# Performance work log

Measured on AMD Instinct MI355X. Metric: run time of the kernel, lower is better.

Reference implementation:

```python
import jax, jax.numpy as jnp
import numpy as np

N_EMB = 512
DIM = 64
BETA = 0.25
EPS = 1e-10


def setup_inputs() -> dict:
    key = jax.random.key(0)
    k1, k2 = jax.random.split(key)
    z = jax.random.normal(k1, (32, 64, 64, 64), dtype=jnp.float32)  # (B, C=DIM, H, W)
    # embedding weight initialized uniform(-1/K, 1/K) as in the module
    weight = jax.random.uniform(k2, (N_EMB, DIM), dtype=jnp.float32,
                                minval=-1.0 / N_EMB, maxval=1.0 / N_EMB)
    return {"z": z, "weight": weight}


def reference(z, weight):
    # (B,C,H,W) -> (B,H,W,C)
    zp = jnp.transpose(z, (0, 2, 3, 1))
    zf = zp.reshape(-1, DIM)  # (N, D)
    # pairwise squared distances ||z||^2 + ||e||^2 - 2 z.e  -> (N, K)
    d = (jnp.sum(zf * zf, axis=1, keepdims=True)
         + jnp.sum(weight * weight, axis=1)
         - 2.0 * zf @ weight.T)
    codebook = jnp.argmin(d, axis=1)  # (N,)
    encodings = jax.nn.one_hot(codebook, N_EMB, dtype=zf.dtype)  # (N, K)
    # direct gather == one_hot @ weight (same math, efficient form)
    z_q = weight[codebook].reshape(zp.shape)
    sg = jax.lax.stop_gradient
    loss = jnp.mean((sg(z_q) - zp) ** 2) + BETA * jnp.mean((z_q - sg(zp)) ** 2)
    # straight-through estimator
    z_q = zp + sg(z_q - zp)
    e_mean = jnp.mean(encodings, axis=0)
    perplexity = jnp.exp(-jnp.sum(e_mean * jnp.log(e_mean + EPS)))
    z_q = jnp.transpose(z_q, (0, 3, 1, 2))  # back to (B,C,H,W)
    return (loss, z_q, perplexity, encodings, codebook)
```

## Files before the change

### kernel.cpp

```cpp
#include <hip/hip_runtime.h>
#include <math.h>

#define NK 512
#define NPTS (32*64*64)
#define NELEM (32*64*64*64)

#define OFF_LOSS 0
#define OFF_ZQ   1
#define OFF_PERP (1 + NELEM)
#define OFF_ENC  (2 + NELEM)
#define OFF_CB   (2 + NELEM + (size_t)NPTS * NK)


__global__ __launch_bounds__(256) void vq_prep(const float* __restrict__ wg,
                                               float* __restrict__ wTT,
                                               float* __restrict__ bnd) {
    __shared__ float tl[64 * 65];
    const int t = threadIdx.x;
    const int kbase = blockIdx.x * 64;
    #pragma unroll
    for (int it = 0; it < 16; ++it) {
        int i = it * 256 + t;
        int k = i >> 6, d = i & 63;
        tl[k * 65 + d] = wg[(size_t)(kbase + k) * 64 + d];
    }
    __syncthreads();
    #pragma unroll
    for (int it = 0; it < 16; ++it) {
        int i = it * 256 + t;
        int kk = i & 63, d = i >> 6;
        int k = kbase + kk;
        wTT[(size_t)((k >> 3) * 64 + d) * 8 + (k & 7)] = tl[kk * 65 + d];
    }
    if (t < 64) {
        float s = 0.f;
        #pragma unroll 4
        for (int d = 0; d < 64; ++d) {
            float v = tl[t * 65 + d];
            s = __fadd_rn(s, __fmul_rn(v, v));
        }
        bnd[kbase + t] = s;
    }
}

__global__ __launch_bounds__(256, 4) void vq_fused(const float* __restrict__ zg,
                                                   const float* __restrict__ wg,
                                                   const float* __restrict__ wTT,
                                                   const float* __restrict__ bndg,
                                                   float* __restrict__ out,
                                                   int* __restrict__ hist,
                                                   double* __restrict__ lossAcc) {
    const int t = threadIdx.x;
    const int wave = t >> 6;
    const int lane = t & 63;
    const int rowInBlk = wave >> 1;
    const int half = wave & 1;
    const int r = blockIdx.x * 2 + rowInBlk;
    const int b = r >> 6;
    const int h = r & 63;
    const size_t base = (size_t)b * 262144 + (size_t)h * 64;

    __shared__ float shv[4][64];
    __shared__ int   shi[4][64];
    __shared__ int   shm[2][64];

    float zreg[64];
    #pragma unroll
    for (int d = 0; d < 64; ++d)
        zreg[d] = zg[base + (size_t)d * 4096 + lane];

    float a = 0.f;
    #pragma unroll
    for (int d = 0; d < 64; ++d)
        a = __fadd_rn(a, __fmul_rn(zreg[d], zreg[d]));

    const int shalf = __builtin_amdgcn_readfirstlane(half);
    const float* wbase = wTT + (size_t)shalf * 32 * 512;
    const float* bnb = bndg + shalf * 256;

    float best = INFINITY;
    int bidx = 0;

    #pragma unroll 1
    for (int cc = 0; cc < 32; ++cc) {
        const float* wrow = wbase + cc * 512;
        float acc[8];
        #pragma unroll
        for (int j = 0; j < 8; ++j) acc[j] = 0.f;

        #pragma unroll
        for (int d = 0; d < 64; ++d) {
            const float zv = zreg[d];
            #pragma unroll
            for (int j = 0; j < 8; ++j)
                acc[j] = fmaf(zv, wrow[d * 8 + j], acc[j]);
        }

        #pragma unroll
        for (int j = 0; j < 8; ++j) {
            float dist = __fsub_rn(__fadd_rn(a, bnb[cc * 8 + j]), 2.0f * acc[j]);
            int k = shalf * 256 + cc * 8 + j;
            if (dist < best) { best = dist; bidx = k; }
        }
    }

    shv[wave][lane] = best;
    shi[wave][lane] = bidx;
    __syncthreads();
    const int w0 = rowInBlk * 2;
    float v0 = shv[w0][lane];     int i0 = shi[w0][lane];
    float v1 = shv[w0 + 1][lane]; int i1 = shi[w0 + 1][lane];
    const int mi = (v1 < v0) ? i1 : i0;

    if (half == 0) {
        shm[rowInBlk][lane] = mi;
        out[OFF_CB + (size_t)r * 64 + lane] = (float)mi;
        atomicAdd(&hist[mi], 1);
    }
    __syncthreads();

    {
        float* encb = out + OFF_ENC + ((size_t)r * 64) * 512;
        const int e0 = lane * 4;
        #pragma unroll 4
        for (int p = 0; p < 32; ++p) {
            int pt = shalf * 32 + p;
            int idx = shm[rowInBlk][pt];
            float* erow = encb + (size_t)pt * 512;
            float4 A, B;
            A.x = (e0 + 0 == idx) ? 1.f : 0.f;
            A.y = (e0 + 1 == idx) ? 1.f : 0.f;
            A.z = (e0 + 2 == idx) ? 1.f : 0.f;
            A.w = (e0 + 3 == idx) ? 1.f : 0.f;
            B.x = (e0 + 256 == idx) ? 1.f : 0.f;
            B.y = (e0 + 257 == idx) ? 1.f : 0.f;
            B.z = (e0 + 258 == idx) ? 1.f : 0.f;
            B.w = (e0 + 259 == idx) ? 1.f : 0.f;
            *(float4*)(erow + e0) = A;
            *(float4*)(erow + 256 + e0) = B;
        }
    }

    float lsum = 0.f;
    {
        const int dlo = shalf * 32;
        const float4* wr4 = (const float4*)(wg + (size_t)mi * 64 + dlo);
        float q[32];
        #pragma unroll
        for (int e = 0; e < 8; ++e) {
            float4 v = wr4[e];
            q[4 * e + 0] = v.x; q[4 * e + 1] = v.y;
            q[4 * e + 2] = v.z; q[4 * e + 3] = v.w;
        }
        float* zq = out + OFF_ZQ + base;
        #pragma unroll
        for (int dd = 0; dd < 32; ++dd) {
            int d = dlo + dd;
            float zv = zreg[d];
            float diff = __fsub_rn(q[dd], zv);
            lsum = __fadd_rn(lsum, __fmul_rn(diff, diff));
            zq[(size_t)d * 4096 + lane] = __fadd_rn(zv, diff);
        }
    }
    #pragma unroll
    for (int off = 32; off > 0; off >>= 1)
        lsum += __shfl_down(lsum, off);
    if (lane == 0)
        atomicAdd(lossAcc, (double)lsum);
}

__global__ __launch_bounds__(512) void vq_finalize(const int* __restrict__ hist,
                                                   const double* __restrict__ lossAcc,
                                                   float* __restrict__ out) {
    __shared__ float sh[512];
    const int t = threadIdx.x;
    float p = (float)hist[t] / (float)NPTS;
    sh[t] = __fmul_rn(p, logf(__fadd_rn(p, 1e-10f)));
    __syncthreads();
    for (int s = 256; s > 0; s >>= 1) {
        if (t < s) sh[t] += sh[t + s];
        __syncthreads();
    }
    if (t == 0) {
        float m = (float)(*lossAcc / (double)NELEM);
        out[OFF_LOSS] = __fadd_rn(m, __fmul_rn(0.25f, m));
        out[OFF_PERP] = expf(-sh[0]);
    }
}

extern "C" void kernel_launch(void* const* d_in, const int* in_sizes, int n_in,
                              void* d_out, int out_size, void* d_ws, size_t ws_size,
                              hipStream_t stream) {
    const float* z = (const float*)d_in[0];
    const float* w = (const float*)d_in[1];
    float* out = (float*)d_out;
    int* hist = (int*)d_ws;
    double* lossAcc = (double*)((char*)d_ws + 2048);
    float* wTT = (float*)((char*)d_ws + 4096);
    float* bnd = wTT + 64 * 512;

    (void)hipMemsetAsync(d_ws, 0, 4096, stream);
    vq_prep<<<8, 256, 0, stream>>>(w, wTT, bnd);
    vq_fused<<<1024, 256, 0, stream>>>(z, w, wTT, bnd, out, hist, lossAcc);
    vq_finalize<<<1, 512, 0, stream>>>(hist, lossAcc, out);
}
```

Baseline: 505.1 us.

## Assign one full image row per wave, dropping cross-wave argmin reduction

Each wave now scans all 512 codes for its 64 points, where before two waves each handled half the codebook and merged results through shared memory. This removes the shared-memory exchange and both block barriers, and broadcasts the indices with wave shuffles when writing the one-hot encodings. The grid is halved and launch bounds relaxed to 2 blocks per SIMD-level occupancy. The trade is fewer resident waves and less parallelism for the compute-heavy distance loop, with a longer serial loop per wave, while the output write phase is reordered to run after the z_q stores.

New measurement: 565.5 us. 1.12x slower.

```diff
diff --git a/kernel.cpp b/kernel.cpp
--- a/kernel.cpp
+++ b/kernel.cpp
@@ -43,7 +43,7 @@
     }
 }
 
-__global__ __launch_bounds__(256, 4) void vq_fused(const float* __restrict__ zg,
+__global__ __launch_bounds__(256, 2) void vq_fused(const float* __restrict__ zg,
                                                    const float* __restrict__ wg,
                                                    const float* __restrict__ wTT,
                                                    const float* __restrict__ bndg,
@@ -53,16 +53,10 @@
     const int t = threadIdx.x;
     const int wave = t >> 6;
     const int lane = t & 63;
-    const int rowInBlk = wave >> 1;
-    const int half = wave & 1;
-    const int r = blockIdx.x * 2 + rowInBlk;
+    const int r = blockIdx.x * 4 + wave;
     const int b = r >> 6;
     const int h = r & 63;
     const size_t base = (size_t)b * 262144 + (size_t)h * 64;
-
-    __shared__ float shv[4][64];
-    __shared__ int   shi[4][64];
-    __shared__ int   shm[2][64];
 
     float zreg[64];
     #pragma unroll
@@ -74,16 +68,12 @@
     for (int d = 0; d < 64; ++d)
         a = __fadd_rn(a, __fmul_rn(zreg[d], zreg[d]));
 
-    const int shalf = __builtin_amdgcn_readfirstlane(half);
-    const float* wbase = wTT + (size_t)shalf * 32 * 512;
-    const float* bnb = bndg + shalf * 256;
-
     float best = INFINITY;
     int bidx = 0;
 
     #pragma unroll 1
-    for (int cc = 0; cc < 32; ++cc) {
-        const float* wrow = wbase + cc * 512;
+    for (int cc = 0; cc < 64; ++cc) {
+        const float* wrow = wTT + cc * 512;
         float acc[8];
         #pragma unroll
         for (int j = 0; j < 8; ++j) acc[j] = 0.f;
@@ -98,35 +88,47 @@
 
         #pragma unroll
         for (int j = 0; j < 8; ++j) {
-            float dist = __fsub_rn(__fadd_rn(a, bnb[cc * 8 + j]), 2.0f * acc[j]);
-            int k = shalf * 256 + cc * 8 + j;
+            float dist = __fsub_rn(__fadd_rn(a, bndg[cc * 8 + j]), 2.0f * acc[j]);
+            int k = cc * 8 + j;
             if (dist < best) { best = dist; bidx = k; }
         }
     }
 
-    shv[wave][lane] = best;
-    shi[wave][lane] = bidx;
-    __syncthreads();
-    const int w0 = rowInBlk * 2;
-    float v0 = shv[w0][lane];     int i0 = shi[w0][lane];
-    float v1 = shv[w0 + 1][lane]; int i1 = shi[w0 + 1][lane];
-    const int mi = (v1 < v0) ? i1 : i0;
+    out[OFF_CB + (size_t)r * 64 + lane] = (float)bidx;
+    atomicAdd(&hist[bidx], 1);
 
-    if (half == 0) {
-        shm[rowInBlk][lane] = mi;
-        out[OFF_CB + (size_t)r * 64 + lane] = (float)mi;
-        atomicAdd(&hist[mi], 1);
+    float lsum = 0.f;
+    {
+        float q[64];
+        const float4* wr4 = (const float4*)(wg + (size_t)bidx * 64);
+        #pragma unroll
+        for (int e = 0; e < 16; ++e) {
+            float4 v = wr4[e];
+            q[4 * e + 0] = v.x; q[4 * e + 1] = v.y;
+            q[4 * e + 2] = v.z; q[4 * e + 3] = v.w;
+        }
+        float* zq = out + OFF_ZQ + base;
+        #pragma unroll
+        for (int d = 0; d < 64; ++d) {
+            float zv = zreg[d];
+            float diff = __fsub_rn(q[d], zv);
+            lsum = __fadd_rn(lsum, __fmul_rn(diff, diff));
+            zq[(size_t)d * 4096 + lane] = __fadd_rn(zv, diff);
+        }
     }
-    __syncthreads();
+    #pragma unroll
+    for (int off = 32; off > 0; off >>= 1)
+        lsum += __shfl_down(lsum, off);
+    if (lane == 0)
+        atomicAdd(lossAcc, (double)lsum);
 
     {
         float* encb = out + OFF_ENC + ((size_t)r * 64) * 512;
         const int e0 = lane * 4;
         #pragma unroll 4
-        for (int p = 0; p < 32; ++p) {
-            int pt = shalf * 32 + p;
-            int idx = shm[rowInBlk][pt];
-            float* erow = encb + (size_t)pt * 512;
+        for (int p = 0; p < 64; ++p) {
+            int idx = __shfl(bidx, p);
+            float* erow = encb + (size_t)p * 512;
             float4 A, B;
             A.x = (e0 + 0 == idx) ? 1.f : 0.f;
             A.y = (e0 + 1 == idx) ? 1.f : 0.f;
@@ -140,33 +142,6 @@
             *(float4*)(erow + 256 + e0) = B;
         }
     }
-
-    float lsum = 0.f;
-    {
-        const int dlo = shalf * 32;
-        const float4* wr4 = (const float4*)(wg + (size_t)mi * 64 + dlo);
-        float q[32];
-        #pragma unroll
-        for (int e = 0; e < 8; ++e) {
-            float4 v = wr4[e];
-            q[4 * e + 0] = v.x; q[4 * e + 1] = v.y;
-            q[4 * e + 2] = v.z; q[4 * e + 3] = v.w;
-        }
-        float* zq = out + OFF_ZQ + base;
-        #pragma unroll
-        for (int dd = 0; dd < 32; ++dd) {
-            int d = dlo + dd;
-            float zv = zreg[d];
-            float diff = __fsub_rn(q[dd], zv);
-            lsum = __fadd_rn(lsum, __fmul_rn(diff, diff));
-            zq[(size_t)d * 4096 + lane] = __fadd_rn(zv, diff);
-        }
-    }
-    #pragma unroll
-    for (int off = 32; off > 0; off >>= 1)
-        lsum += __shfl_down(lsum, off);
-    if (lane == 0)
-        atomicAdd(lossAcc, (double)lsum);
 }
 
 __global__ __launch_bounds__(512) void vq_finalize(const int* __restrict__ hist,
@@ -201,6 +176,6 @@
 
     (void)hipMemsetAsync(d_ws, 0, 4096, stream);
     vq_prep<<<8, 256, 0, stream>>>(w, wTT, bnd);
-    vq_fused<<<1024, 256, 0, stream>>>(z, w, wTT, bnd, out, hist, lossAcc);
+    vq_fused<<<512, 256, 0, stream>>>(z, w, wTT, bnd, out, hist, lossAcc);
     vq_finalize<<<1, 512, 0, stream>>>(hist, lossAcc, out);
 }
```
